# Kernel tuning notes

Hardware: AMD Instinct MI355X
Metric: run time of the kernel (lower is better)

The kernel has to match this reference:

```python
import jax, jax.numpy as jnp
import numpy as np

N_HEADS = 8
HEAD_D = 64


def setup_inputs() -> dict:
    key = jax.random.key(0)
    ks = jax.random.split(key, 7)
    b, ds, dc = 4, 4096, 256
    ls, lc = 512, 512
    inner = N_HEADS * HEAD_D  # 512
    out_dim = 512
    data = jax.random.normal(ks[0], (b, ds, dc), dtype=jnp.float32)
    latent = jax.random.normal(ks[1], (b, ls, lc), dtype=jnp.float32)
    # torch nn.Linear weights are [out_features, in_features]
    Wq = jax.random.normal(ks[2], (inner, lc), dtype=jnp.float32) * (lc ** -0.5)
    Wk = jax.random.normal(ks[3], (inner, dc), dtype=jnp.float32) * (dc ** -0.5)
    Wv = jax.random.normal(ks[4], (inner, dc), dtype=jnp.float32) * (dc ** -0.5)
    Wo = jax.random.normal(ks[5], (out_dim, inner), dtype=jnp.float32) * (inner ** -0.5)
    bo = jax.random.normal(ks[6], (out_dim,), dtype=jnp.float32) * 0.02
    return {"data": data, "latent": latent, "Wq": Wq, "Wk": Wk, "Wv": Wv, "Wo": Wo, "bo": bo}


def reference(data, latent, Wq, Wk, Wv, Wo, bo):
    b, ds, _ = data.shape
    ls = latent.shape[1]
    scale = HEAD_D ** -0.5
    # projections, split into heads
    Q = (latent @ Wq.T).reshape(b, ls, N_HEADS, HEAD_D)  # [b,ls,h,d]
    K = (data @ Wk.T).reshape(b, ds, N_HEADS, HEAD_D)    # [b,ds,h,d]
    V = (data @ Wv.T).reshape(b, ds, N_HEADS, HEAD_D)
    # logits [b, ds, ls, h]; original broadcasts then sums over head_d -> einsum
    logits = jnp.einsum('blhd,bshd->bslh', Q, K) * scale
    # softmax over key axis (dim 1 = ds), matching attn_logits.softmax(1)
    attn = jax.nn.softmax(logits, axis=1)
    # weighted sum over keys: [b, ls, h, d] -> [b, ls, inner]
    out = jnp.einsum('bshd,bslh->blhd', V, attn).reshape(b, ls, N_HEADS * HEAD_D)
    # output Linear (dropout is identity in eval)
    return out @ Wo.T + bo
```

## Files before the change

kernel.cpp:

```cpp
#include <hip/hip_runtime.h>

typedef __bf16 bf16;
typedef __bf16 bf16x4 __attribute__((ext_vector_type(4)));
typedef __bf16 bf16x8 __attribute__((ext_vector_type(8)));
typedef float  f32x4  __attribute__((ext_vector_type(4)));


__device__ __forceinline__ bf16x8 cvt8(float4 a, float4 b) {
    bf16x8 r;
    r[0] = (bf16)a.x; r[1] = (bf16)a.y; r[2] = (bf16)a.z; r[3] = (bf16)a.w;
    r[4] = (bf16)b.x; r[5] = (bf16)b.y; r[6] = (bf16)b.z; r[7] = (bf16)b.w;
    return r;
}

__device__ __forceinline__ void gload16(const bf16* g, bf16* l) {
    __builtin_amdgcn_global_load_lds(
        (const __attribute__((address_space(1))) unsigned int*)(g),
        (__attribute__((address_space(3))) unsigned int*)(l), 16, 0, 0);
}

__global__ __launch_bounds__(256) void cvt_in(
    const float* __restrict__ data, const float* __restrict__ latent,
    const float* __restrict__ Wq, const float* __restrict__ Wk,
    const float* __restrict__ Wv, const float* __restrict__ Wo,
    bf16* __restrict__ db, bf16* __restrict__ lb, bf16* __restrict__ qb,
    bf16* __restrict__ kb, bf16* __restrict__ vb, bf16* __restrict__ ob)
{
    const int bx = blockIdx.x;
    const float* src; bf16* dst; float scale = 1.0f; int base;
    if      (bx < 2048) { src = data;   dst = db; base = bx; }
    else if (bx < 2560) { src = latent; dst = lb; base = bx - 2048; }
    else if (bx < 2688) { src = Wq;     dst = qb; base = bx - 2560; scale = 0.125f; }
    else if (bx < 2752) { src = Wk;     dst = kb; base = bx - 2688; }
    else if (bx < 2816) { src = Wv;     dst = vb; base = bx - 2752; }
    else                { src = Wo;     dst = ob; base = bx - 2816; }
    size_t off = (size_t)base * 2048 + (size_t)threadIdx.x * 8;
    float4 a = *(const float4*)(src + off);
    float4 b = *(const float4*)(src + off + 4);
    a.x *= scale; a.y *= scale; a.z *= scale; a.w *= scale;
    b.x *= scale; b.y *= scale; b.z *= scale; b.w *= scale;
    *(bf16x8*)(dst + off) = cvt8(a, b);
}

#define LDT 136
__global__ __launch_bounds__(256) void proj_kvq(
    const bf16* __restrict__ data, const bf16* __restrict__ latent,
    const bf16* __restrict__ Wk, const bf16* __restrict__ Wv, const bf16* __restrict__ Wq,
    bf16* __restrict__ K_b, bf16* __restrict__ Vt_b, bf16* __restrict__ Q_b)
{
    __shared__ __align__(16) bf16 arena[24576];

    const int bx = blockIdx.x;
    const int tid = threadIdx.x;
    const int wave = tid >> 6, lane = tid & 63;
    const int wm = wave >> 1, wn = wave & 1;
    const int l15 = lane & 15, quad = lane >> 4;
    const int rowS = wave * 32 + (lane >> 2);
    const int colS = (lane & 3) * 8;

    if (bx >= 64) {
        const int t = bx - 64;
        const int m0 = (t & 127) * 128, n0 = (t >> 7) * 128;

        const bf16* Asrc = data + (size_t)(m0 + rowS) * 256 + colS;
        const bf16* Ksrc = Wk   + (size_t)(n0 + rowS) * 256 + colS;
        const bf16* Vsrc = Wv   + (size_t)(n0 + rowS) * 256 + colS;

        f32x4 accK[4][4] = {}, accV[4][4] = {};

#define STAGE_KV(buf, k0) do { \
        bf16* Lb = arena + (buf) * 12288 + wave * 1024; \
        gload16(Asrc + (k0),        Lb);          \
        gload16(Asrc + (k0) + 4096, Lb + 512);    \
        gload16(Ksrc + (k0),        Lb + 4096);   \
        gload16(Ksrc + (k0) + 4096, Lb + 4608);   \
        gload16(Vsrc + (k0),        Lb + 8192);   \
        gload16(Vsrc + (k0) + 4096, Lb + 8704);   \
    } while (0)

        STAGE_KV(0, 0);
        asm volatile("s_waitcnt vmcnt(0)" ::: "memory");
        __syncthreads();
        int cur = 0;
        for (int k0 = 0; k0 < 256; k0 += 32) {
            if (k0 + 32 < 256) STAGE_KV(cur ^ 1, k0 + 32);
            const bf16* B = arena + cur * 12288;

            bf16x8 af[4];
            #pragma unroll
            for (int mt = 0; mt < 4; mt++)
                af[mt] = *(const bf16x8*)(B + (wm * 64 + mt * 16 + l15) * 32 + quad * 8);
            #pragma unroll
            for (int nt = 0; nt < 4; nt++) {
                bf16x8 bk = *(const bf16x8*)(B + 4096 + (wn * 64 + nt * 16 + l15) * 32 + quad * 8);
                #pragma unroll
                for (int mt = 0; mt < 4; mt++)
                    accK[mt][nt] = __builtin_amdgcn_mfma_f32_16x16x32_bf16(af[mt], bk, accK[mt][nt], 0, 0, 0);
            }
            #pragma unroll
            for (int nt = 0; nt < 4; nt++) {
                bf16x8 bv = *(const bf16x8*)(B + 8192 + (wn * 64 + nt * 16 + l15) * 32 + quad * 8);
                #pragma unroll
                for (int mt = 0; mt < 4; mt++)
                    accV[mt][nt] = __builtin_amdgcn_mfma_f32_16x16x32_bf16(af[mt], bv, accV[mt][nt], 0, 0, 0);
            }
            __syncthreads();
            cur ^= 1;
        }
#undef STAGE_KV

        #pragma unroll
        for (int mt = 0; mt < 4; mt++)
            #pragma unroll
            for (int nt = 0; nt < 4; nt++)
                #pragma unroll
                for (int r = 0; r < 4; r++) {
                    int ml = wm * 64 + mt * 16 + quad * 4 + r;
                    int nl = wn * 64 + nt * 16 + l15;
                    arena[ml * LDT + nl] = (bf16)accK[mt][nt][r];
                }
        __syncthreads();
        #pragma unroll
        for (int c = 0; c < 8; c++) {
            int idx = c * 256 + tid;
            int row = idx >> 4, col = (idx & 15) * 8;
            bf16x8 vv = *(const bf16x8*)(arena + row * LDT + col);
            int m = m0 + row, n = n0 + col;
            *(bf16x8*)(K_b + (size_t)((m >> 12) * 8 + (n >> 6)) * 262144 + (m & 4095) * 64 + (n & 63)) = vv;
        }
        __syncthreads();
        #pragma unroll
        for (int mt = 0; mt < 4; mt++)
            #pragma unroll
            for (int nt = 0; nt < 4; nt++)
                #pragma unroll
                for (int r = 0; r < 4; r++) {
                    int ml = wm * 64 + mt * 16 + quad * 4 + r;
                    int nl = wn * 64 + nt * 16 + l15;
                    arena[nl * LDT + ml] = (bf16)accV[mt][nt][r];
                }
        __syncthreads();
        #pragma unroll
        for (int c = 0; c < 8; c++) {
            int idx = c * 256 + tid;
            int row = idx >> 4, col = (idx & 15) * 8;
            bf16x8 vv = *(const bf16x8*)(arena + row * LDT + col);
            int d = n0 + row, s = m0 + col;
            *(bf16x8*)(Vt_b + (size_t)((s >> 12) * 8 + (d >> 6)) * 262144 + (d & 63) * 4096 + (s & 4095)) = vv;
        }
    } else {
        const int m0 = (bx & 15) * 128, n0 = (bx >> 4) * 128;

        const bf16* Asrc = latent + (size_t)(m0 + rowS) * 512 + colS;
        const bf16* Bsrc = Wq     + (size_t)(n0 + rowS) * 512 + colS;

        f32x4 acc[4][4] = {};

#define STAGE_Q(buf, k0) do { \
        bf16* Lb = arena + (buf) * 8192 + wave * 1024; \
        gload16(Asrc + (k0),        Lb);          \
        gload16(Asrc + (k0) + 8192, Lb + 512);    \
        gload16(Bsrc + (k0),        Lb + 4096);   \
        gload16(Bsrc + (k0) + 8192, Lb + 4608);   \
    } while (0)

        STAGE_Q(0, 0);
        asm volatile("s_waitcnt vmcnt(0)" ::: "memory");
        __syncthreads();
        int cur = 0;
        for (int k0 = 0; k0 < 512; k0 += 32) {
            if (k0 + 32 < 512) STAGE_Q(cur ^ 1, k0 + 32);
            const bf16* B = arena + cur * 8192;

            bf16x8 af[4], bfr[4];
            #pragma unroll
            for (int mt = 0; mt < 4; mt++)
                af[mt] = *(const bf16x8*)(B + (wm * 64 + mt * 16 + l15) * 32 + quad * 8);
            #pragma unroll
            for (int nt = 0; nt < 4; nt++)
                bfr[nt] = *(const bf16x8*)(B + 4096 + (wn * 64 + nt * 16 + l15) * 32 + quad * 8);
            #pragma unroll
            for (int mt = 0; mt < 4; mt++)
                #pragma unroll
                for (int nt = 0; nt < 4; nt++)
                    acc[mt][nt] = __builtin_amdgcn_mfma_f32_16x16x32_bf16(af[mt], bfr[nt], acc[mt][nt], 0, 0, 0);
            __syncthreads();
            cur ^= 1;
        }
#undef STAGE_Q

        #pragma unroll
        for (int mt = 0; mt < 4; mt++)
            #pragma unroll
            for (int nt = 0; nt < 4; nt++)
                #pragma unroll
                for (int r = 0; r < 4; r++) {
                    int ml = wm * 64 + mt * 16 + quad * 4 + r;
                    int nl = wn * 64 + nt * 16 + l15;
                    arena[ml * LDT + nl] = (bf16)acc[mt][nt][r];
                }
        __syncthreads();
        #pragma unroll
        for (int c = 0; c < 8; c++) {
            int idx = c * 256 + tid;
            int row = idx >> 4, col = (idx & 15) * 8;
            bf16x8 vv = *(const bf16x8*)(arena + row * LDT + col);
            int m = m0 + row, n = n0 + col;
            *(bf16x8*)(Q_b + (size_t)((m >> 9) * 8 + (n >> 6)) * 32768 + (m & 511) * 64 + (n & 63)) = vv;
        }
    }
}

#define LDK 72
#define LDP 72
__global__ __launch_bounds__(256) void flash_attn(
    const bf16* __restrict__ Q, const bf16* __restrict__ K,
    const bf16* __restrict__ Vt, float* __restrict__ Opart, float* __restrict__ lbuf)
{
    __shared__ bf16 Ks[64 * LDK];
    __shared__ bf16 Vs[64 * LDK];
    __shared__ bf16 Ps[4][2 * 16 * LDP];

    const int tid = threadIdx.x;
    const int bx = blockIdx.x;
    const int qt = bx >> 7;
    const int bh = (bx & 127) >> 2;
    const int ks = bx & 3;
    const int wave = tid >> 6, lane = tid & 63;
    const int l15 = lane & 15, quad = lane >> 4;

    const bf16* Qb = Q + (size_t)bh * 32768 + (size_t)(qt * 128 + wave * 32 + l15) * 64;
    bf16x8 aq[2][2];
    aq[0][0] = *(const bf16x8*)(Qb + quad * 8);
    aq[0][1] = *(const bf16x8*)(Qb + 32 + quad * 8);
    aq[1][0] = *(const bf16x8*)(Qb + 1024 + quad * 8);
    aq[1][1] = *(const bf16x8*)(Qb + 1024 + 32 + quad * 8);

    const bf16* Kb = K + (size_t)bh * 262144;
    const bf16* Vb = Vt + (size_t)bh * 262144;

    f32x4 oacc[2][4] = {};
    float lsum[2] = {0.f, 0.f};

    const int i0 = tid, i1 = tid + 256;
    const int r0 = i0 >> 3, c0 = (i0 & 7) * 8;
    const int r1 = i1 >> 3, c1 = (i1 & 7) * 8;

    const int kstart = ks * 1024, kend = kstart + 1024;

    uint4 pk0 = *(const uint4*)(Kb + (size_t)(kstart + r0) * 64 + c0);
    uint4 pk1 = *(const uint4*)(Kb + (size_t)(kstart + r1) * 64 + c1);
    uint4 pv0 = *(const uint4*)(Vb + (size_t)r0 * 4096 + kstart + c0);
    uint4 pv1 = *(const uint4*)(Vb + (size_t)r1 * 4096 + kstart + c1);

    bf16* Pw = &Ps[wave][0];

    for (int key0 = kstart; key0 < kend; key0 += 64) {
        __syncthreads();
        *(uint4*)(Ks + r0 * LDK + c0) = pk0;
        *(uint4*)(Ks + r1 * LDK + c1) = pk1;
        *(uint4*)(Vs + r0 * LDK + c0) = pv0;
        *(uint4*)(Vs + r1 * LDK + c1) = pv1;
        if (key0 + 64 < kend) {
            pk0 = *(const uint4*)(Kb + (size_t)(key0 + 64 + r0) * 64 + c0);
            pk1 = *(const uint4*)(Kb + (size_t)(key0 + 64 + r1) * 64 + c1);
            pv0 = *(const uint4*)(Vb + (size_t)r0 * 4096 + key0 + 64 + c0);
            pv1 = *(const uint4*)(Vb + (size_t)r1 * 4096 + key0 + 64 + c1);
        }
        __syncthreads();

        __builtin_amdgcn_s_setprio(1);
        #pragma unroll
        for (int mt = 0; mt < 4; mt++) {
            bf16x8 bk0 = *(const bf16x8*)(Ks + (mt * 16 + l15) * LDK + quad * 8);
            bf16x8 bk1 = *(const bf16x8*)(Ks + (mt * 16 + l15) * LDK + 32 + quad * 8);
            #pragma unroll
            for (int u = 0; u < 2; u++) {
                f32x4 z = {};
                z = __builtin_amdgcn_mfma_f32_16x16x32_bf16(bk0, aq[u][0], z, 0, 0, 0);
                z = __builtin_amdgcn_mfma_f32_16x16x32_bf16(bk1, aq[u][1], z, 0, 0, 0);
                bf16x4 pv4;
                float s = 0.f;
                #pragma unroll
                for (int r = 0; r < 4; r++) {
                    float e = __expf(z[r]);
                    s += e;
                    pv4[r] = (bf16)e;
                }
                lsum[u] += s;
                *(bf16x4*)(Pw + u * 16 * LDP + l15 * LDP + mt * 16 + quad * 4) = pv4;
            }
        }
        __builtin_amdgcn_s_setprio(0);

        bf16x8 ap[2][2];
        #pragma unroll
        for (int u = 0; u < 2; u++) {
            ap[u][0] = *(const bf16x8*)(Pw + u * 16 * LDP + l15 * LDP + quad * 8);
            ap[u][1] = *(const bf16x8*)(Pw + u * 16 * LDP + l15 * LDP + 32 + quad * 8);
        }
        __builtin_amdgcn_s_setprio(1);
        #pragma unroll
        for (int dt = 0; dt < 4; dt++) {
            bf16x8 bv0 = *(const bf16x8*)(Vs + (dt * 16 + l15) * LDK + quad * 8);
            bf16x8 bv1 = *(const bf16x8*)(Vs + (dt * 16 + l15) * LDK + 32 + quad * 8);
            #pragma unroll
            for (int u = 0; u < 2; u++) {
                oacc[u][dt] = __builtin_amdgcn_mfma_f32_16x16x32_bf16(ap[u][0], bv0, oacc[u][dt], 0, 0, 0);
                oacc[u][dt] = __builtin_amdgcn_mfma_f32_16x16x32_bf16(ap[u][1], bv1, oacc[u][dt], 0, 0, 0);
            }
        }
        __builtin_amdgcn_s_setprio(0);
    }

    #pragma unroll
    for (int u = 0; u < 2; u++) {
        lsum[u] += __shfl_xor(lsum[u], 16, 64);
        lsum[u] += __shfl_xor(lsum[u], 32, 64);
    }

    #pragma unroll
    for (int u = 0; u < 2; u++) {
        const int rowbase = bh * 512 + qt * 128 + wave * 32 + u * 16 + quad * 4;
        #pragma unroll
        for (int dt = 0; dt < 4; dt++) {
            #pragma unroll
            for (int r = 0; r < 4; r++) {
                Opart[((size_t)ks * 16384 + rowbase + r) * 64 + dt * 16 + l15] = oacc[u][dt][r];
            }
        }
        if (quad == 0) {
            lbuf[(size_t)ks * 16384 + bh * 512 + qt * 128 + wave * 32 + u * 16 + l15] = lsum[u];
        }
    }
}

__global__ __launch_bounds__(256) void merge_o(
    const float* __restrict__ Opart, const float* __restrict__ lbuf, bf16* __restrict__ O)
{
    const int idx = blockIdx.x * 256 + threadIdx.x;
    const int row = idx >> 3;
    const int d0 = (idx & 7) * 8;
    float L = 0.f;
    float4 s0 = {0,0,0,0}, s1 = {0,0,0,0};
    #pragma unroll
    for (int ks = 0; ks < 4; ks++) {
        L += lbuf[(size_t)ks * 16384 + row];
        float4 p0 = *(const float4*)(Opart + ((size_t)ks * 16384 + row) * 64 + d0);
        float4 p1 = *(const float4*)(Opart + ((size_t)ks * 16384 + row) * 64 + d0 + 4);
        s0.x += p0.x; s0.y += p0.y; s0.z += p0.z; s0.w += p0.w;
        s1.x += p1.x; s1.y += p1.y; s1.z += p1.z; s1.w += p1.w;
    }
    float inv = 1.0f / L;
    s0.x *= inv; s0.y *= inv; s0.z *= inv; s0.w *= inv;
    s1.x *= inv; s1.y *= inv; s1.z *= inv; s1.w *= inv;
    const int bh = row >> 9, l = row & 511;
    const int b = bh >> 3, h = bh & 7;
    *(bf16x8*)(O + ((size_t)(b * 512 + l)) * 512 + h * 64 + d0) = cvt8(s0, s1);
}

__global__ __launch_bounds__(256) void gemm_out(
    const bf16* __restrict__ O, const bf16* __restrict__ Wo_b,
    const float* __restrict__ bo, float* __restrict__ out)
{
    __shared__ bf16 As[2048];
    __shared__ bf16 Bs[2048];
    const int tid = threadIdx.x;
    const int m0 = blockIdx.x * 64, n0 = blockIdx.y * 64;
    const int wave = tid >> 6, lane = tid & 63;
    const int wm = wave >> 1, wn = wave & 1;
    const int l15 = lane & 15, quad = lane >> 4;
    const int rowA = tid >> 2;
    const int c8 = (tid & 3) * 8;

    f32x4 acc[2][2] = {};
    bf16x8 pa = *(const bf16x8*)(O    + (size_t)(m0 + rowA) * 512 + c8);
    bf16x8 pb = *(const bf16x8*)(Wo_b + (size_t)(n0 + rowA) * 512 + c8);

    for (int k0 = 0; k0 < 512; k0 += 32) {
        __syncthreads();
        *(bf16x8*)(As + (size_t)tid * 8) = pa;
        *(bf16x8*)(Bs + (size_t)tid * 8) = pb;
        if (k0 + 32 < 512) {
            pa = *(const bf16x8*)(O    + (size_t)(m0 + rowA) * 512 + k0 + 32 + c8);
            pb = *(const bf16x8*)(Wo_b + (size_t)(n0 + rowA) * 512 + k0 + 32 + c8);
        }
        __syncthreads();

        bf16x8 af[2], bfr[2];
        #pragma unroll
        for (int mt = 0; mt < 2; mt++)
            af[mt] = *(const bf16x8*)(As + (wm * 32 + mt * 16 + l15) * 32 + quad * 8);
        #pragma unroll
        for (int nt = 0; nt < 2; nt++)
            bfr[nt] = *(const bf16x8*)(Bs + (wn * 32 + nt * 16 + l15) * 32 + quad * 8);
        #pragma unroll
        for (int mt = 0; mt < 2; mt++)
            #pragma unroll
            for (int nt = 0; nt < 2; nt++)
                acc[mt][nt] = __builtin_amdgcn_mfma_f32_16x16x32_bf16(af[mt], bfr[nt], acc[mt][nt], 0, 0, 0);
    }

    #pragma unroll
    for (int mt = 0; mt < 2; mt++) {
        #pragma unroll
        for (int nt = 0; nt < 2; nt++) {
            #pragma unroll
            for (int r = 0; r < 4; r++) {
                int mm = m0 + wm * 32 + mt * 16 + quad * 4 + r;
                int nn = n0 + wn * 32 + nt * 16 + l15;
                out[(size_t)mm * 512 + nn] = acc[mt][nt][r] + bo[nn];
            }
        }
    }
}

extern "C" void kernel_launch(void* const* d_in, const int* in_sizes, int n_in,
                              void* d_out, int out_size, void* d_ws, size_t ws_size,
                              hipStream_t stream) {
    const float* data   = (const float*)d_in[0];
    const float* latent = (const float*)d_in[1];
    const float* Wq = (const float*)d_in[2];
    const float* Wk = (const float*)d_in[3];
    const float* Wv = (const float*)d_in[4];
    const float* Wo = (const float*)d_in[5];
    const float* bo = (const float*)d_in[6];
    float* out = (float*)d_out;

    bf16* ws = (bf16*)d_ws;
    bf16* Q_b    = ws;
    bf16* K_b    = Q_b + 1048576;
    bf16* Vt_b   = K_b + 8388608;
    float* Opart = (float*)(Vt_b + 8388608);
    float* lbuf  = Opart + 4 * 16384 * 64;
    bf16* data_bf = (bf16*)(lbuf + 4 * 16384);
    bf16* lat_bf  = data_bf + 4194304;
    bf16* Wq_bf   = lat_bf + 1048576;
    bf16* Wk_bf   = Wq_bf + 262144;
    bf16* Wv_bf   = Wk_bf + 131072;
    bf16* Wo_bf   = Wv_bf + 131072;
    bf16* O_bf    = Wo_bf + 262144;

    cvt_in<<<2944, 256, 0, stream>>>(data, latent, Wq, Wk, Wv, Wo,
                                     data_bf, lat_bf, Wq_bf, Wk_bf, Wv_bf, Wo_bf);
    proj_kvq<<<576, 256, 0, stream>>>(data_bf, lat_bf, Wk_bf, Wv_bf, Wq_bf, K_b, Vt_b, Q_b);
    flash_attn<<<512, 256, 0, stream>>>(Q_b, K_b, Vt_b, Opart, lbuf);
    merge_o<<<512, 256, 0, stream>>>(Opart, lbuf, O_bf);
    gemm_out<<<dim3(32, 8), 256, 0, stream>>>(O_bf, Wo_bf, bo, out);
}
```

Before: 135.2 us.

## Switch flash attention to 32x32 MFMA with in-register P via permlane swap

Reworks the attention inner loop to use 32x32x16 bf16 MFMA tiles instead of 16x16x32, computing S as K*Q^T so the exp'd probabilities land in registers in a layout that, after v_permlane32_swap, directly feeds the PV MFMA. This drops the per-wave LDS round-trip for P and its shared buffer. It also changes the K/V LDS padding to a row-group skewed offset to avoid bank conflicts with the new access pattern, and uses packed bf16 conversion instructions. It relies on gfx950-specific instructions and on a correct fragment mapping, which is intricate.

```diff
diff --git a/kernel.cpp b/kernel.cpp
--- a/kernel.cpp
+++ b/kernel.cpp
@@ -4,6 +4,7 @@
 typedef __bf16 bf16x4 __attribute__((ext_vector_type(4)));
 typedef __bf16 bf16x8 __attribute__((ext_vector_type(8)));
 typedef float  f32x4  __attribute__((ext_vector_type(4)));
+typedef float  f32x16 __attribute__((ext_vector_type(16)));
 
 
 __device__ __forceinline__ bf16x8 cvt8(float4 a, float4 b) {
@@ -211,15 +212,14 @@
     }
 }
 
-#define LDK 72
-#define LDP 72
+__device__ __forceinline__ int kvoff(int r, int c) { return r * 72 + ((r >> 3) << 3) + c; }
+
 __global__ __launch_bounds__(256) void flash_attn(
     const bf16* __restrict__ Q, const bf16* __restrict__ K,
     const bf16* __restrict__ Vt, float* __restrict__ Opart, float* __restrict__ lbuf)
 {
-    __shared__ bf16 Ks[64 * LDK];
-    __shared__ bf16 Vs[64 * LDK];
-    __shared__ bf16 Ps[4][2 * 16 * LDP];
+    __shared__ __align__(16) bf16 Ks[4672];
+    __shared__ __align__(16) bf16 Vs[4672];
 
     const int tid = threadIdx.x;
     const int bx = blockIdx.x;
@@ -227,24 +227,24 @@
     const int bh = (bx & 127) >> 2;
     const int ks = bx & 3;
     const int wave = tid >> 6, lane = tid & 63;
-    const int l15 = lane & 15, quad = lane >> 4;
-
-    const bf16* Qb = Q + (size_t)bh * 32768 + (size_t)(qt * 128 + wave * 32 + l15) * 64;
-    bf16x8 aq[2][2];
-    aq[0][0] = *(const bf16x8*)(Qb + quad * 8);
-    aq[0][1] = *(const bf16x8*)(Qb + 32 + quad * 8);
-    aq[1][0] = *(const bf16x8*)(Qb + 1024 + quad * 8);
-    aq[1][1] = *(const bf16x8*)(Qb + 1024 + 32 + quad * 8);
+    const int q32 = lane & 31;
+    const int hi = lane >> 5;
+
+    const bf16* Qrow = Q + (size_t)bh * 32768 + (size_t)(qt * 128 + wave * 32 + q32) * 64 + hi * 8;
+    bf16x8 qf[4];
+    #pragma unroll
+    for (int c = 0; c < 4; c++) qf[c] = *(const bf16x8*)(Qrow + c * 16);
 
     const bf16* Kb = K + (size_t)bh * 262144;
     const bf16* Vb = Vt + (size_t)bh * 262144;
 
-    f32x4 oacc[2][4] = {};
-    float lsum[2] = {0.f, 0.f};
+    f32x16 oacc[2] = {};
+    float lsum = 0.f;
 
     const int i0 = tid, i1 = tid + 256;
     const int r0 = i0 >> 3, c0 = (i0 & 7) * 8;
     const int r1 = i1 >> 3, c1 = (i1 & 7) * 8;
+    const int ko0 = kvoff(r0, c0), ko1 = kvoff(r1, c1);
 
     const int kstart = ks * 1024, kend = kstart + 1024;
 
@@ -253,14 +253,12 @@
     uint4 pv0 = *(const uint4*)(Vb + (size_t)r0 * 4096 + kstart + c0);
     uint4 pv1 = *(const uint4*)(Vb + (size_t)r1 * 4096 + kstart + c1);
 
-    bf16* Pw = &Ps[wave][0];
-
     for (int key0 = kstart; key0 < kend; key0 += 64) {
         __syncthreads();
-        *(uint4*)(Ks + r0 * LDK + c0) = pk0;
-        *(uint4*)(Ks + r1 * LDK + c1) = pk1;
-        *(uint4*)(Vs + r0 * LDK + c0) = pv0;
-        *(uint4*)(Vs + r1 * LDK + c1) = pv1;
+        *(uint4*)(Ks + ko0) = pk0;
+        *(uint4*)(Ks + ko1) = pk1;
+        *(uint4*)(Vs + ko0) = pv0;
+        *(uint4*)(Vs + ko1) = pv1;
         if (key0 + 64 < kend) {
             pk0 = *(const uint4*)(Kb + (size_t)(key0 + 64 + r0) * 64 + c0);
             pk1 = *(const uint4*)(Kb + (size_t)(key0 + 64 + r1) * 64 + c1);
@@ -271,68 +269,52 @@
 
         __builtin_amdgcn_s_setprio(1);
         #pragma unroll
-        for (int mt = 0; mt < 4; mt++) {
-            bf16x8 bk0 = *(const bf16x8*)(Ks + (mt * 16 + l15) * LDK + quad * 8);
-            bf16x8 bk1 = *(const bf16x8*)(Ks + (mt * 16 + l15) * LDK + 32 + quad * 8);
-            #pragma unroll
-            for (int u = 0; u < 2; u++) {
-                f32x4 z = {};
-                z = __builtin_amdgcn_mfma_f32_16x16x32_bf16(bk0, aq[u][0], z, 0, 0, 0);
-                z = __builtin_amdgcn_mfma_f32_16x16x32_bf16(bk1, aq[u][1], z, 0, 0, 0);
-                bf16x4 pv4;
-                float s = 0.f;
-                #pragma unroll
-                for (int r = 0; r < 4; r++) {
-                    float e = __expf(z[r]);
-                    s += e;
-                    pv4[r] = (bf16)e;
+        for (int khalf = 0; khalf < 2; khalf++) {
+            f32x16 z = {};
+            #pragma unroll
+            for (int c4 = 0; c4 < 4; c4++) {
+                bf16x8 kf = *(const bf16x8*)(Ks + kvoff(khalf * 32 + q32, c4 * 16 + hi * 8));
+                z = __builtin_amdgcn_mfma_f32_32x32x16_bf16(kf, qf[c4], z, 0, 0, 0);
+            }
+            unsigned w0[4], w1[4];
+            #pragma unroll
+            for (int o = 0; o < 4; o++) {
+                float p0 = __expf(z[4 * o]),     p1 = __expf(z[4 * o + 1]);
+                float p2 = __expf(z[4 * o + 2]), p3 = __expf(z[4 * o + 3]);
+                lsum += (p0 + p1) + (p2 + p3);
+                asm("v_cvt_pk_bf16_f32 %0, %1, %2" : "=v"(w0[o]) : "v"(p0), "v"(p1));
+                asm("v_cvt_pk_bf16_f32 %0, %1, %2" : "=v"(w1[o]) : "v"(p2), "v"(p3));
+            }
+            #pragma unroll
+            for (int c = 0; c < 2; c++) {
+                unsigned a0 = w0[2 * c], b0 = w0[2 * c + 1];
+                unsigned a1 = w1[2 * c], b1 = w1[2 * c + 1];
+                asm("v_permlane32_swap_b32 %0, %1" : "+v"(a0), "+v"(b0));
+                asm("v_permlane32_swap_b32 %0, %1" : "+v"(a1), "+v"(b1));
+                uint4 fr; fr.x = a0; fr.y = a1; fr.z = b0; fr.w = b1;
+                bf16x8 pf = *(bf16x8*)&fr;
+                #pragma unroll
+                for (int dt = 0; dt < 2; dt++) {
+                    bf16x8 vf = *(const bf16x8*)(Vs + kvoff(dt * 32 + q32, khalf * 32 + c * 16 + hi * 8));
+                    oacc[dt] = __builtin_amdgcn_mfma_f32_32x32x16_bf16(pf, vf, oacc[dt], 0, 0, 0);
                 }
-                lsum[u] += s;
-                *(bf16x4*)(Pw + u * 16 * LDP + l15 * LDP + mt * 16 + quad * 4) = pv4;
             }
         }
         __builtin_amdgcn_s_setprio(0);
-
-        bf16x8 ap[2][2];
-        #pragma unroll
-        for (int u = 0; u < 2; u++) {
-            ap[u][0] = *(const bf16x8*)(Pw + u * 16 * LDP + l15 * LDP + quad * 8);
-            ap[u][1] = *(const bf16x8*)(Pw + u * 16 * LDP + l15 * LDP + 32 + quad * 8);
-        }
-        __builtin_amdgcn_s_setprio(1);
-        #pragma unroll
-        for (int dt = 0; dt < 4; dt++) {
-            bf16x8 bv0 = *(const bf16x8*)(Vs + (dt * 16 + l15) * LDK + quad * 8);
-            bf16x8 bv1 = *(const bf16x8*)(Vs + (dt * 16 + l15) * LDK + 32 + quad * 8);
-            #pragma unroll
-            for (int u = 0; u < 2; u++) {
-                oacc[u][dt] = __builtin_amdgcn_mfma_f32_16x16x32_bf16(ap[u][0], bv0, oacc[u][dt], 0, 0, 0);
-                oacc[u][dt] = __builtin_amdgcn_mfma_f32_16x16x32_bf16(ap[u][1], bv1, oacc[u][dt], 0, 0, 0);
-            }
-        }
-        __builtin_amdgcn_s_setprio(0);
-    }
-
+    }
+
+    lsum += __shfl_xor(lsum, 32, 64);
+
+    const int rowbase = bh * 512 + qt * 128 + wave * 32;
     #pragma unroll
-    for (int u = 0; u < 2; u++) {
-        lsum[u] += __shfl_xor(lsum[u], 16, 64);
-        lsum[u] += __shfl_xor(lsum[u], 32, 64);
-    }
-
-    #pragma unroll
-    for (int u = 0; u < 2; u++) {
-        const int rowbase = bh * 512 + qt * 128 + wave * 32 + u * 16 + quad * 4;
-        #pragma unroll
-        for (int dt = 0; dt < 4; dt++) {
-            #pragma unroll
-            for (int r = 0; r < 4; r++) {
-                Opart[((size_t)ks * 16384 + rowbase + r) * 64 + dt * 16 + l15] = oacc[u][dt][r];
-            }
-        }
-        if (quad == 0) {
-            lbuf[(size_t)ks * 16384 + bh * 512 + qt * 128 + wave * 32 + u * 16 + l15] = lsum[u];
-        }
-    }
+    for (int dt = 0; dt < 2; dt++) {
+        #pragma unroll
+        for (int r = 0; r < 16; r++) {
+            int q = (r & 3) + 8 * (r >> 2) + 4 * hi;
+            Opart[((size_t)ks * 16384 + rowbase + q) * 64 + dt * 32 + q32] = oacc[dt][r];
+        }
+    }
+    if (lane < 32) lbuf[(size_t)ks * 16384 + rowbase + lane] = lsum;
 }
 
 __global__ __launch_bounds__(256) void merge_o(
```

Measured after the change: 136.2 us. About the same (+0.7%).
